# Kernel optimization log

Measured on AMD Instinct MI355X. Metric: run time of the kernel, lower is better.

## Reference

```python
import jax, jax.numpy as jnp
import numpy as np
from jax import lax

GROUPS = 32
EPS = 1e-5
NEG_SLOPE = 0.1


def group_norm(x, gamma, beta):
    # x: (B, C, H, W); GroupNorm over (C//G, H, W) per group
    B, C, H, W = x.shape
    xr = x.reshape(B, GROUPS, C // GROUPS, H, W)
    mean = xr.mean(axis=(2, 3, 4), keepdims=True)
    var = xr.var(axis=(2, 3, 4), keepdims=True)
    xn = ((xr - mean) * lax.rsqrt(var + EPS)).reshape(B, C, H, W)
    return xn * gamma[None, :, None, None] + beta[None, :, None, None]


def conv3x3(x, w, b):
    y = lax.conv_general_dilated(x, w, (1, 1), 'SAME',
                                 dimension_numbers=('NCHW', 'OIHW', 'NCHW'))
    return y + b[None, :, None, None]


def leaky_relu(x):
    return jnp.where(x >= 0, x, NEG_SLOPE * x)


def setup_inputs() -> dict:
    key = jax.random.key(0)
    ks = jax.random.split(key, 12)
    B, C, H, W = 16, 128, 128, 128
    emb = 128
    s = 0.05
    return {
        'x': jax.random.normal(ks[0], (B, C, H, W), jnp.float32),
        'time_emb': jax.random.normal(ks[1], (B, emb), jnp.float32),
        'k_v': jax.random.normal(ks[2], (B, 64), jnp.float32),
        'gn1_g': jnp.ones((C,), jnp.float32),
        'gn1_b': jnp.zeros((C,), jnp.float32),
        'conv1_w': jax.random.normal(ks[3], (C, C, 3, 3), jnp.float32) * s,
        'conv1_b': jax.random.normal(ks[4], (C,), jnp.float32) * s,
        'nf_w': jax.random.normal(ks[5], (C, emb), jnp.float32) * s,
        'nf_b': jax.random.normal(ks[6], (C,), jnp.float32) * s,
        'kW1': jax.random.normal(ks[7], (64, 64), jnp.float32) * s,
        'kW2': jax.random.normal(ks[8], (C * 9, 64), jnp.float32) * s,
        'daconv_w': jax.random.normal(ks[9], (C, C, 3, 3), jnp.float32) * s,
        'daconv_b': jax.random.normal(ks[10], (C,), jnp.float32) * s,
    }


def reference(x, time_emb, k_v, gn1_g, gn1_b, conv1_w, conv1_b,
              nf_w, nf_b, kW1, kW2, daconv_w, daconv_b):
    B, C, H, W = x.shape
    # block1: GroupNorm -> Swish -> Conv3x3
    h = group_norm(x, gn1_g, gn1_b)
    h = h * jax.nn.sigmoid(h)
    h = conv3x3(h, conv1_w, conv1_b)
    # FeatureWiseAffine (use_affine_level=False): h + Linear(time_emb)
    h = h + (time_emb @ nf_w.T + nf_b)[:, :, None, None]
    # DABlock: its GroupNorm+Swish output is discarded in the original code,
    # so only DA_conv(h, k_v) matters.
    # dynamic per-sample depthwise kernel: (B, 64) -> (B*C, 1, 3, 3)
    kern = (leaky_relu(k_v @ kW1.T) @ kW2.T).reshape(B * C, 1, 3, 3)
    xr = h.reshape(1, B * C, H, W)
    dyn = lax.conv_general_dilated(xr, kern, (1, 1), 'SAME',
                                   dimension_numbers=('NCHW', 'OIHW', 'NCHW'),
                                   feature_group_count=B * C)
    dyn = leaky_relu(dyn).reshape(B, C, H, W)
    h = dyn + conv3x3(h, daconv_w, daconv_b)
    # residual: dim == dim_out -> res_conv = Identity
    return h + x
```

## Files before the change

kernel.cpp:

```cpp
#include <hip/hip_runtime.h>
#include <hip/hip_bf16.h>
#include <math.h>
#include <stdint.h>

typedef unsigned short u16;
typedef __attribute__((ext_vector_type(8))) short bfrag;
typedef __attribute__((ext_vector_type(4))) float f32x4;
typedef __attribute__((ext_vector_type(8))) unsigned short u16x8;
typedef __attribute__((ext_vector_type(4))) unsigned short u16x4;

#define BB 16
#define CC 128
#define HH 128
#define WW 128
#define EPSV 1e-5f
#define NEG 0.1f
#define PW 130

__device__ __forceinline__ float bf2f(u16 u) {
    unsigned int x = ((unsigned int)u) << 16;
    return __builtin_bit_cast(float, x);
}
__device__ __forceinline__ u16 f2bf(float f) {
    unsigned int x = __builtin_bit_cast(unsigned int, f);
    unsigned int r = x + 0x7fffu + ((x >> 16) & 1u);
    return (u16)(r >> 16);
}
__device__ __forceinline__ void gload_lds16(const void* g, void* l) {
    __builtin_amdgcn_global_load_lds(
        (const __attribute__((address_space(1))) void*)g,
        (__attribute__((address_space(3))) void*)l, 16, 0, 0);
}

__global__ __launch_bounds__(256)
void border_kernel(u16* __restrict__ a, u16* __restrict__ h) {
    int idx = blockIdx.x * 256 + threadIdx.x;
    if (idx >= BB * 516 * 16) return;
    int cg = idx & 15;
    int t = idx >> 4;
    int b = t / 516, e = t - b * 516;
    int y, x;
    if (e < 130)      { y = 0;           x = e; }
    else if (e < 260) { y = 129;         x = e - 130; }
    else if (e < 388) { y = e - 260 + 1; x = 0; }
    else              { y = e - 388 + 1; x = 129; }
    size_t o = (((size_t)b * PW + y) * PW + x) * 128 + cg * 8;
    u16x8 z = (u16x8)(u16)0;
    *(u16x8*)&a[o] = z;
    *(u16x8*)&h[o] = z;
}

__global__ __launch_bounds__(256)
void gn_stats_kernel(const float* __restrict__ x, float* __restrict__ stats) {
    const int bg = blockIdx.x;
    const float* base = x + (size_t)bg * 65536;
    float s1 = 0.f, s2 = 0.f;
    for (int i = threadIdx.x; i < 16384; i += 256) {
        float4 v = *(const float4*)&base[i * 4];
        s1 += v.x + v.y + v.z + v.w;
        s2 += v.x * v.x + v.y * v.y + v.z * v.z + v.w * v.w;
    }
    #pragma unroll
    for (int off = 32; off > 0; off >>= 1) {
        s1 += __shfl_down(s1, off);
        s2 += __shfl_down(s2, off);
    }
    __shared__ float rs[8];
    const int wid = threadIdx.x >> 6, lane = threadIdx.x & 63;
    if (lane == 0) { rs[wid * 2] = s1; rs[wid * 2 + 1] = s2; }
    __syncthreads();
    if (threadIdx.x == 0) {
        s1 = rs[0] + rs[2] + rs[4] + rs[6];
        s2 = rs[1] + rs[3] + rs[5] + rs[7];
        float mean = s1 * (1.f / 65536.f);
        float var  = s2 * (1.f / 65536.f) - mean * mean;
        stats[2 * bg]     = mean;
        stats[2 * bg + 1] = rsqrtf(var + EPSV);
    }
}

__global__ __launch_bounds__(256)
void wconv_kernel(const float* __restrict__ w1, const float* __restrict__ w2,
                  u16* __restrict__ w1t, u16* __restrict__ w2t) {
    int idx = blockIdx.x * 256 + threadIdx.x;
    if (idx < 147456) {
        int e  = idx & 7;
        int co = (idx >> 3) & 127;
        int g  = (idx >> 10) & 3;
        int ck = (idx >> 12) & 3;
        int t  = idx >> 14;
        int src = (co * 128 + (ck * 32 + g * 8 + e)) * 9 + t;
        w1t[idx] = f2bf(w1[src]);
        w2t[idx] = f2bf(w2[src]);
    }
}

__global__ __launch_bounds__(256)
void small1_kernel(const float* __restrict__ te, const float* __restrict__ nfw,
                   const float* __restrict__ nfbias, const float* __restrict__ c1b,
                   const float* __restrict__ kv, const float* __restrict__ kw1,
                   float* __restrict__ biastot, float* __restrict__ tmp1) {
    const int idx = blockIdx.x * 256 + threadIdx.x;
    if (idx < 1024) {
        const int b = idx >> 6, j = idx & 63;
        float s = 0.f;
        for (int e = 0; e < 64; ++e) s += kv[b * 64 + e] * kw1[j * 64 + e];
        tmp1[idx] = s >= 0.f ? s : NEG * s;
    } else if (idx < 1024 + 2048) {
        const int t = idx - 1024;
        const int b = t >> 7, c = t & 127;
        float s = nfbias[c] + c1b[c];
        for (int e = 0; e < 128; ++e) s += te[b * 128 + e] * nfw[c * 128 + e];
        biastot[t] = s;
    }
}

__global__ __launch_bounds__(256)
void small2_kernel(const float* __restrict__ tmp1, const float* __restrict__ kw2,
                   float* __restrict__ kern_t) {
    const int idx = blockIdx.x * 256 + threadIdx.x;
    if (idx < BB * CC * 9) {
        const int b = idx / 1152, rc = idx % 1152;
        const int c = rc / 9, t = rc - c * 9;
        float s = 0.f;
        for (int e = 0; e < 64; ++e) s += tmp1[b * 64 + e] * kw2[rc * 64 + e];
        kern_t[((size_t)b * 9 + t) * 128 + c] = s;
    }
}

__global__ __launch_bounds__(256)
void gn_apply_kernel(const float* __restrict__ x, const float* __restrict__ gamma,
                     const float* __restrict__ beta, const float* __restrict__ stats,
                     u16* __restrict__ hact) {
    __shared__ u16 s_t[128 * 128];
    const int tid = threadIdx.x;
    const int y = blockIdx.x & 127, b = blockIdx.x >> 7;
    #pragma unroll
    for (int i = 0; i < 16; ++i) {
        int unit = (i << 8) + tid;
        int c = unit >> 5, xq = unit & 31, xx = xq * 4;
        float4 v = *(const float4*)&x[(((size_t)b * 128 + c) * 128 + y) * 128 + xx];
        int gi = b * 32 + (c >> 2);
        float mean = stats[2 * gi], rstd = stats[2 * gi + 1];
        float ga = gamma[c] * rstd, be = beta[c] - mean * ga;
        float a0 = v.x * ga + be, a1 = v.y * ga + be, a2 = v.z * ga + be, a3 = v.w * ga + be;
        a0 = a0 / (1.f + __expf(-a0)); a1 = a1 / (1.f + __expf(-a1));
        a2 = a2 / (1.f + __expf(-a2)); a3 = a3 / (1.f + __expf(-a3));
        int cs = c ^ ((xq & 15) << 3);
        s_t[(xx + 0) * 128 + cs] = f2bf(a0);
        s_t[(xx + 1) * 128 + cs] = f2bf(a1);
        s_t[(xx + 2) * 128 + cs] = f2bf(a2);
        s_t[(xx + 3) * 128 + cs] = f2bf(a3);
    }
    __syncthreads();
    #pragma unroll
    for (int i = 0; i < 8; ++i) {
        int unit = (i << 8) + tid;
        int xx = unit >> 4, c0 = (unit & 15) * 8;
        int c0s = c0 ^ (((xx >> 2) & 15) << 3);
        u16x8 v = *(const u16x8*)&s_t[xx * 128 + c0s];
        *(u16x8*)&hact[(((size_t)b * PW + y + 1) * PW + (xx + 1)) * 128 + c0] = v;
    }
}

template <int FINAL>
__global__ __launch_bounds__(512, 2)
void conv_mfma_kernel(const u16* __restrict__ act, const u16* __restrict__ wt,
                      const float* __restrict__ bias, const float* __restrict__ kern_t,
                      const float* __restrict__ xres,
                      float* __restrict__ outf, u16* __restrict__ outh) {
    __shared__ __align__(16) u16 s_in[2][1536 * 8];
    __shared__ float s_k[1152];

    const int tid = threadIdx.x;
    const int lane = tid & 63, wid = tid >> 6;
    const int wm = wid & 1, wq = wid >> 1;
    const int l15 = lane & 15, l4 = lane >> 4;

    const int bid0 = blockIdx.x;
    const int bid = ((bid0 & 7) << 7) | (bid0 >> 3);
    const int tx = bid & 7, ty = (bid >> 3) & 7, b = bid >> 6;
    const int x0 = tx * 16, y0 = ty * 16;

    f32x4 acc[4][4];
    #pragma unroll
    for (int mi = 0; mi < 4; ++mi)
        #pragma unroll
        for (int nj = 0; nj < 4; ++nj) acc[mi][nj] = (f32x4)(0.f);

    float dw[2][2][4][4];
    if constexpr (FINAL) {
        #pragma unroll
        for (int a0 = 0; a0 < 2; ++a0)
            #pragma unroll
            for (int a1 = 0; a1 < 2; ++a1)
                #pragma unroll
                for (int a2 = 0; a2 < 4; ++a2)
                    #pragma unroll
                    for (int a3 = 0; a3 < 4; ++a3) dw[a0][a1][a2][a3] = 0.f;
        for (int i = tid; i < 1152; i += 512) s_k[i] = kern_t[(size_t)b * 1152 + i];
        __syncthreads();
    }

    int in_vofs[3];
    #pragma unroll
    for (int r = 0; r < 3; ++r) {
        int slot = r * 512 + tid;
        int cik = slot / 384;
        int pos = slot - cik * 384;
        if (pos > 323) pos = 323;
        int row = pos / 18, col = pos - row * 18;
        in_vofs[r] = (row * PW + col) * 128 + cik * 8;
    }
    const u16* in_base = act + (((size_t)b * PW + y0) * PW + x0) * 128;
    const int ldst = (wid << 6) * 8;

    auto stage_in = [&](int buf, int ci0) {
        #pragma unroll
        for (int r = 0; r < 3; ++r)
            gload_lds16(in_base + ci0 + in_vofs[r], &s_in[buf][r * 512 * 8 + ldst]);
    };

    const u16* wlane = wt + l4 * 1024 + (wm * 64 + l15) * 8;
    const int bbase = (l4 * 384 + (wq * 4) * 18 + l15) * 8;

    auto dwcomp = [&](int ck, int dyr) {
        if constexpr (FINAL) {
            if ((ck >> 1) == wm) {
                const int mih = ck & 1;
                const u16* sb = &s_in[ck & 1][0];
                #pragma unroll
                for (int mm = 0; mm < 2; ++mm) {
                    const int cik = 2 * mm + (l4 >> 1);
                    const int e0 = (l4 & 1) * 4;
                    const int cb = ck * 32 + mm * 16 + l4 * 4;
                    #pragma unroll
                    for (int dx = 0; dx < 3; ++dx) {
                        const int tap = dyr * 3 + dx;
                        float4 kk = *(const float4*)&s_k[tap * 128 + cb];
                        #pragma unroll
                        for (int nj = 0; nj < 4; ++nj) {
                            const int row = wq * 4 + nj + dyr;
                            const int col = l15 + dx;
                            u16x4 hv = *(const u16x4*)
                                &sb[(cik * 384 + row * 18 + col) * 8 + e0];
                            dw[mih][mm][nj][0] += bf2f(hv[0]) * kk.x;
                            dw[mih][mm][nj][1] += bf2f(hv[1]) * kk.y;
                            dw[mih][mm][nj][2] += bf2f(hv[2]) * kk.z;
                            dw[mih][mm][nj][3] += bf2f(hv[3]) * kk.w;
                        }
                    }
                }
            }
        }
    };

    stage_in(0, 0);
    asm volatile("s_waitcnt vmcnt(0)" ::: "memory");
    __builtin_amdgcn_s_barrier();
    __builtin_amdgcn_sched_barrier(0);

    #pragma unroll
    for (int c = 0; c < 4; ++c) {
        if (c > 0) {
            __builtin_amdgcn_s_barrier();
        }
        if (c < 3) {
            stage_in((c + 1) & 1, (c + 1) * 32);
            asm volatile("s_waitcnt vmcnt(3)" ::: "memory");
        }
        __builtin_amdgcn_sched_barrier(0);

        const u16* sb = &s_in[c & 1][0];
        #pragma unroll
        for (int dyr = 0; dyr < 3; ++dyr) {
            bfrag wR[3][4];
            #pragma unroll
            for (int dx = 0; dx < 3; ++dx) {
                const u16* wp = wlane + ((dyr * 3 + dx) * 4 + c) * 4096;
                #pragma unroll
                for (int mi = 0; mi < 4; ++mi)
                    wR[dx][mi] = *(const bfrag*)(wp + mi * 128);
            }
            __builtin_amdgcn_s_setprio(1);
            #pragma unroll
            for (int dx = 0; dx < 3; ++dx) {
                const int bo = bbase + (dyr * 18 + dx) * 8;
                bfrag b0 = *(const bfrag*)&sb[bo];
                bfrag b1 = *(const bfrag*)&sb[bo + 144];
                bfrag b2 = *(const bfrag*)&sb[bo + 288];
                bfrag b3 = *(const bfrag*)&sb[bo + 432];

                acc[0][0] = __builtin_amdgcn_mfma_f32_16x16x32_bf16(wR[dx][0], b0, acc[0][0], 0, 0, 0);
                acc[0][1] = __builtin_amdgcn_mfma_f32_16x16x32_bf16(wR[dx][0], b1, acc[0][1], 0, 0, 0);
                acc[0][2] = __builtin_amdgcn_mfma_f32_16x16x32_bf16(wR[dx][0], b2, acc[0][2], 0, 0, 0);
                acc[0][3] = __builtin_amdgcn_mfma_f32_16x16x32_bf16(wR[dx][0], b3, acc[0][3], 0, 0, 0);
                acc[1][0] = __builtin_amdgcn_mfma_f32_16x16x32_bf16(wR[dx][1], b0, acc[1][0], 0, 0, 0);
                acc[1][1] = __builtin_amdgcn_mfma_f32_16x16x32_bf16(wR[dx][1], b1, acc[1][1], 0, 0, 0);
                acc[1][2] = __builtin_amdgcn_mfma_f32_16x16x32_bf16(wR[dx][1], b2, acc[1][2], 0, 0, 0);
                acc[1][3] = __builtin_amdgcn_mfma_f32_16x16x32_bf16(wR[dx][1], b3, acc[1][3], 0, 0, 0);
                acc[2][0] = __builtin_amdgcn_mfma_f32_16x16x32_bf16(wR[dx][2], b0, acc[2][0], 0, 0, 0);
                acc[2][1] = __builtin_amdgcn_mfma_f32_16x16x32_bf16(wR[dx][2], b1, acc[2][1], 0, 0, 0);
                acc[2][2] = __builtin_amdgcn_mfma_f32_16x16x32_bf16(wR[dx][2], b2, acc[2][2], 0, 0, 0);
                acc[2][3] = __builtin_amdgcn_mfma_f32_16x16x32_bf16(wR[dx][2], b3, acc[2][3], 0, 0, 0);
                acc[3][0] = __builtin_amdgcn_mfma_f32_16x16x32_bf16(wR[dx][3], b0, acc[3][0], 0, 0, 0);
                acc[3][1] = __builtin_amdgcn_mfma_f32_16x16x32_bf16(wR[dx][3], b1, acc[3][1], 0, 0, 0);
                acc[3][2] = __builtin_amdgcn_mfma_f32_16x16x32_bf16(wR[dx][3], b2, acc[3][2], 0, 0, 0);
                acc[3][3] = __builtin_amdgcn_mfma_f32_16x16x32_bf16(wR[dx][3], b3, acc[3][3], 0, 0, 0);
            }
            __builtin_amdgcn_s_setprio(0);
            dwcomp(c, dyr);
        }
    }

    if (!FINAL) {
        const float* bb = bias + b * 128;
        #pragma unroll
        for (int mi = 0; mi < 4; ++mi) {
            const int cb = wm * 64 + mi * 16 + l4 * 4;
            float4 bv4 = *(const float4*)&bb[cb];
            #pragma unroll
            for (int nj = 0; nj < 4; ++nj) {
                int y = y0 + wq * 4 + nj, xx = x0 + l15;
                u16x4 pk;
                pk[0] = f2bf(acc[mi][nj][0] + bv4.x);
                pk[1] = f2bf(acc[mi][nj][1] + bv4.y);
                pk[2] = f2bf(acc[mi][nj][2] + bv4.z);
                pk[3] = f2bf(acc[mi][nj][3] + bv4.w);
                *(u16x4*)&outh[(((size_t)b * PW + y + 1) * PW + (xx + 1)) * 128 + cb] = pk;
            }
        }
    } else {
        #pragma unroll
        for (int mi = 0; mi < 4; ++mi) {
            const int cb = wm * 64 + mi * 16 + l4 * 4;
            float4 bv4 = *(const float4*)&bias[cb];
            #pragma unroll
            for (int nj = 0; nj < 4; ++nj) {
                int y = y0 + wq * 4 + nj, xx = x0 + l15;
                size_t obase = (((size_t)b * 128 + cb) * 128 + y) * 128 + xx;
                #pragma unroll
                for (int j = 0; j < 4; ++j) {
                    float d = dw[mi >> 1][mi & 1][nj][j];
                    d = d >= 0.f ? d : NEG * d;
                    float bj = (j == 0) ? bv4.x : (j == 1) ? bv4.y : (j == 2) ? bv4.z : bv4.w;
                    outf[obase + (size_t)j * 16384] =
                        acc[mi][nj][j] + bj + d + xres[obase + (size_t)j * 16384];
                }
            }
        }
    }
}

extern "C" void kernel_launch(void* const* d_in, const int* in_sizes, int n_in,
                              void* d_out, int out_size, void* d_ws, size_t ws_size,
                              hipStream_t stream) {
    const float* x        = (const float*)d_in[0];
    const float* te       = (const float*)d_in[1];
    const float* kv       = (const float*)d_in[2];
    const float* gn1_g    = (const float*)d_in[3];
    const float* gn1_b    = (const float*)d_in[4];
    const float* conv1_w  = (const float*)d_in[5];
    const float* conv1_b  = (const float*)d_in[6];
    const float* nf_w     = (const float*)d_in[7];
    const float* nf_b     = (const float*)d_in[8];
    const float* kW1      = (const float*)d_in[9];
    const float* kW2      = (const float*)d_in[10];
    const float* daconv_w = (const float*)d_in[11];
    const float* daconv_b = (const float*)d_in[12];

    float* out = (float*)d_out;

    float* kern  = (float*)d_ws;
    u16*   w2t   = (u16*)(kern + 18432);
    u16*   hbuf  = (u16*)(kern + 92160);

    u16*   hact    = (u16*)out;
    float* up      = out + 17500160;
    float* stats   = up;
    float* biastot = up + 1024;
    float* tmp1    = up + 3072;
    u16*   w1t     = (u16*)(up + 4096);

    border_kernel<<<dim3(516), dim3(256), 0, stream>>>(hact, hbuf);
    gn_stats_kernel<<<dim3(512), dim3(256), 0, stream>>>(x, stats);
    wconv_kernel<<<dim3(576), dim3(256), 0, stream>>>(conv1_w, daconv_w, w1t, w2t);
    small1_kernel<<<dim3(12), dim3(256), 0, stream>>>(te, nf_w, nf_b, conv1_b, kv, kW1,
                                                      biastot, tmp1);
    small2_kernel<<<dim3(72), dim3(256), 0, stream>>>(tmp1, kW2, kern);
    gn_apply_kernel<<<dim3(2048), dim3(256), 0, stream>>>(x, gn1_g, gn1_b, stats, hact);

    conv_mfma_kernel<0><<<dim3(1024), dim3(512), 0, stream>>>(
        hact, w1t, biastot, nullptr, nullptr, nullptr, hbuf);
    conv_mfma_kernel<1><<<dim3(1024), dim3(512), 0, stream>>>(
        hbuf, w2t, daconv_b, kern, x, out, nullptr);
}
```

Baseline: 316.0 us.

## Split conv kernels and give conv1 taller 32-row tiles with 1024-thread blocks

Replaces the templated conv kernel with two separate kernels. conv1 now uses 1024-thread blocks, each covering a 32x16 spatial tile, so the 3x3 halo rows are reloaded less often relative to the output area. It reads weight fragments straight from global memory for every tap. conv2 keeps the original tiling and dynamic depthwise fusion, with some dead index code. The larger tile raises LDS use per block, and the aggressive launch bounds may limit registers and occupancy.

```diff
diff --git a/kernel.cpp b/kernel.cpp
--- a/kernel.cpp
+++ b/kernel.cpp
@@ -163,14 +163,10 @@
     }
 }
 
-template <int FINAL>
-__global__ __launch_bounds__(512, 2)
-void conv_mfma_kernel(const u16* __restrict__ act, const u16* __restrict__ wt,
-                      const float* __restrict__ bias, const float* __restrict__ kern_t,
-                      const float* __restrict__ xres,
-                      float* __restrict__ outf, u16* __restrict__ outh) {
-    __shared__ __align__(16) u16 s_in[2][1536 * 8];
-    __shared__ float s_k[1152];
+__global__ __launch_bounds__(1024, 4)
+void conv1_mfma_kernel(const u16* __restrict__ act, const u16* __restrict__ wt,
+                       const float* __restrict__ bias, u16* __restrict__ outh) {
+    __shared__ __align__(16) u16 s_in[2][2496 * 8];
 
     const int tid = threadIdx.x;
     const int lane = tid & 63, wid = tid >> 6;
@@ -178,9 +174,131 @@
     const int l15 = lane & 15, l4 = lane >> 4;
 
     const int bid0 = blockIdx.x;
+    const int bid = ((bid0 & 7) << 6) | (bid0 >> 3);
+    const int tx = bid & 7, ty = (bid >> 3) & 3, b = bid >> 5;
+    const int x0 = tx * 16, y0 = ty * 32;
+
+    f32x4 acc[4][4];
+    #pragma unroll
+    for (int mi = 0; mi < 4; ++mi)
+        #pragma unroll
+        for (int nj = 0; nj < 4; ++nj) acc[mi][nj] = (f32x4)(0.f);
+
+    int in_vofs[3];
+    bool in_act[3];
+    #pragma unroll
+    for (int r = 0; r < 3; ++r) {
+        int slot_base = r * 1024 + (wid << 6);
+        in_act[r] = slot_base < 2448;
+        int slot = r * 1024 + tid;
+        if (slot > 2447) slot = 2447;
+        int cik = slot / 612;
+        int pos = slot - cik * 612;
+        int row = pos / 18, col = pos - row * 18;
+        in_vofs[r] = (row * PW + col) * 128 + cik * 8;
+    }
+    const u16* in_base = act + (((size_t)b * PW + y0) * PW + x0) * 128;
+    const int ldst = (wid << 6) * 8;
+
+    auto stage_in = [&](int buf, int ci0) {
+        #pragma unroll
+        for (int r = 0; r < 3; ++r)
+            if (in_act[r])
+                gload_lds16(in_base + ci0 + in_vofs[r],
+                            &s_in[buf][(r * 1024) * 8 + ldst]);
+    };
+
+    const u16* wlane = wt + l4 * 1024 + (wm * 64 + l15) * 8;
+    const int bbase = (l4 * 612 + (wq * 4) * 18 + l15) * 8;
+
+    stage_in(0, 0);
+    asm volatile("s_waitcnt vmcnt(0)" ::: "memory");
+    __builtin_amdgcn_s_barrier();
+    __builtin_amdgcn_sched_barrier(0);
+
+    #pragma unroll
+    for (int c = 0; c < 4; ++c) {
+        if (c > 0) {
+            asm volatile("s_waitcnt vmcnt(0)" ::: "memory");
+            __builtin_amdgcn_s_barrier();
+        }
+        if (c < 3) stage_in((c + 1) & 1, (c + 1) * 32);
+        __builtin_amdgcn_sched_barrier(0);
+
+        const u16* sb = &s_in[c & 1][0];
+        #pragma unroll
+        for (int dyr = 0; dyr < 3; ++dyr) {
+            #pragma unroll
+            for (int dx = 0; dx < 3; ++dx) {
+                const u16* wp = wlane + ((dyr * 3 + dx) * 4 + c) * 4096;
+                bfrag a0 = *(const bfrag*)(wp);
+                bfrag a1 = *(const bfrag*)(wp + 128);
+                bfrag a2 = *(const bfrag*)(wp + 256);
+                bfrag a3 = *(const bfrag*)(wp + 384);
+                const int bo = bbase + (dyr * 18 + dx) * 8;
+                bfrag b0 = *(const bfrag*)&sb[bo];
+                bfrag b1 = *(const bfrag*)&sb[bo + 144];
+                bfrag b2 = *(const bfrag*)&sb[bo + 288];
+                bfrag b3 = *(const bfrag*)&sb[bo + 432];
+
+                __builtin_amdgcn_s_setprio(1);
+                acc[0][0] = __builtin_amdgcn_mfma_f32_16x16x32_bf16(a0, b0, acc[0][0], 0, 0, 0);
+                acc[0][1] = __builtin_amdgcn_mfma_f32_16x16x32_bf16(a0, b1, acc[0][1], 0, 0, 0);
+                acc[0][2] = __builtin_amdgcn_mfma_f32_16x16x32_bf16(a0, b2, acc[0][2], 0, 0, 0);
+                acc[0][3] = __builtin_amdgcn_mfma_f32_16x16x32_bf16(a0, b3, acc[0][3], 0, 0, 0);
+                acc[1][0] = __builtin_amdgcn_mfma_f32_16x16x32_bf16(a1, b0, acc[1][0], 0, 0, 0);
+                acc[1][1] = __builtin_amdgcn_mfma_f32_16x16x32_bf16(a1, b1, acc[1][1], 0, 0, 0);
+                acc[1][2] = __builtin_amdgcn_mfma_f32_16x16x32_bf16(a1, b2, acc[1][2], 0, 0, 0);
+                acc[1][3] = __builtin_amdgcn_mfma_f32_16x16x32_bf16(a1, b3, acc[1][3], 0, 0, 0);
+                acc[2][0] = __builtin_amdgcn_mfma_f32_16x16x32_bf16(a2, b0, acc[2][0], 0, 0, 0);
+                acc[2][1] = __builtin_amdgcn_mfma_f32_16x16x32_bf16(a2, b1, acc[2][1], 0, 0, 0);
+                acc[2][2] = __builtin_amdgcn_mfma_f32_16x16x32_bf16(a2, b2, acc[2][2], 0, 0, 0);
+                acc[2][3] = __builtin_amdgcn_mfma_f32_16x16x32_bf16(a2, b3, acc[2][3], 0, 0, 0);
+                acc[3][0] = __builtin_amdgcn_mfma_f32_16x16x32_bf16(a3, b0, acc[3][0], 0, 0, 0);
+                acc[3][1] = __builtin_amdgcn_mfma_f32_16x16x32_bf16(a3, b1, acc[3][1], 0, 0, 0);
+                acc[3][2] = __builtin_amdgcn_mfma_f32_16x16x32_bf16(a3, b2, acc[3][2], 0, 0, 0);
+                acc[3][3] = __builtin_amdgcn_mfma_f32_16x16x32_bf16(a3, b3, acc[3][3], 0, 0, 0);
+                __builtin_amdgcn_s_setprio(0);
+            }
+        }
+    }
+
+    const float* bb = bias + b * 128;
+    #pragma unroll
+    for (int mi = 0; mi < 4; ++mi) {
+        const int cb = wm * 64 + mi * 16 + l4 * 4;
+        float4 bv4 = *(const float4*)&bb[cb];
+        #pragma unroll
+        for (int nj = 0; nj < 4; ++nj) {
+            int y = y0 + wq * 4 + nj, xx = x0 + l15;
+            u16x4 pk;
+            pk[0] = f2bf(acc[mi][nj][0] + bv4.x);
+            pk[1] = f2bf(acc[mi][nj][1] + bv4.y);
+            pk[2] = f2bf(acc[mi][nj][2] + bv4.z);
+            pk[3] = f2bf(acc[mi][nj][3] + bv4.w);
+            *(u16x4*)&outh[(((size_t)b * PW + y + 1) * PW + (xx + 1)) * 128 + cb] = pk;
+        }
+    }
+}
+
+__global__ __launch_bounds__(512, 2)
+void conv2_mfma_kernel(const u16* __restrict__ act, const u16* __restrict__ wt,
+                       const float* __restrict__ bias, const float* __restrict__ kern_t,
+                       const float* __restrict__ xres, float* __restrict__ outf) {
+    __shared__ __align__(16) u16 s_in[2][1536 * 8];
+    __shared__ float s_k[1152];
+
+    const int tid = threadIdx.x;
+    const int lane = tid & 63, wid = tid >> 6;
+    const int wm = wid & 1, wq = wid >> 1;
+    const int l15 = lane & 15, l4 = lane >> 4;
+
+    const int bid0 = blockIdx.x;
     const int bid = ((bid0 & 7) << 7) | (bid0 >> 3);
-    const int tx = bid & 7, ty = (bid >> 3) & 7, b = bid >> 6;
-    const int x0 = tx * 16, y0 = ty * 16;
+    const int tx = bid & 7, ty = (bid >> 3) & 15, b = bid >> 7;
+    const int x0 = tx * 16, y0 = (ty & 7) * 16;
+    const int b2 = bid >> 6;
+    (void)b2;
 
     f32x4 acc[4][4];
     #pragma unroll
@@ -189,18 +307,22 @@
         for (int nj = 0; nj < 4; ++nj) acc[mi][nj] = (f32x4)(0.f);
 
     float dw[2][2][4][4];
-    if constexpr (FINAL) {
-        #pragma unroll
-        for (int a0 = 0; a0 < 2; ++a0)
-            #pragma unroll
-            for (int a1 = 0; a1 < 2; ++a1)
+    #pragma unroll
+    for (int a0 = 0; a0 < 2; ++a0)
+        #pragma unroll
+        for (int a1 = 0; a1 < 2; ++a1)
+            #pragma unroll
+            for (int a2 = 0; a2 < 4; ++a2)
                 #pragma unroll
-                for (int a2 = 0; a2 < 4; ++a2)
-                    #pragma unroll
-                    for (int a3 = 0; a3 < 4; ++a3) dw[a0][a1][a2][a3] = 0.f;
-        for (int i = tid; i < 1152; i += 512) s_k[i] = kern_t[(size_t)b * 1152 + i];
-        __syncthreads();
-    }
+                for (int a3 = 0; a3 < 4; ++a3) dw[a0][a1][a2][a3] = 0.f;
+
+    const int bb_ = bid >> 6;
+    const int b_  = bb_;
+    const int ty_ = (bid >> 3) & 7;
+    const int y0_ = ty_ * 16;
+
+    for (int i = tid; i < 1152; i += 512) s_k[i] = kern_t[(size_t)b_ * 1152 + i];
+    __syncthreads();
 
     int in_vofs[3];
     #pragma unroll
@@ -212,7 +334,7 @@
         int row = pos / 18, col = pos - row * 18;
         in_vofs[r] = (row * PW + col) * 128 + cik * 8;
     }
-    const u16* in_base = act + (((size_t)b * PW + y0) * PW + x0) * 128;
+    const u16* in_base = act + (((size_t)b_ * PW + y0_) * PW + x0) * 128;
     const int ldst = (wid << 6) * 8;
 
     auto stage_in = [&](int buf, int ci0) {
@@ -225,30 +347,28 @@
     const int bbase = (l4 * 384 + (wq * 4) * 18 + l15) * 8;
 
     auto dwcomp = [&](int ck, int dyr) {
-        if constexpr (FINAL) {
-            if ((ck >> 1) == wm) {
-                const int mih = ck & 1;
-                const u16* sb = &s_in[ck & 1][0];
+        if ((ck >> 1) == wm) {
+            const int mih = ck & 1;
+            const u16* sb = &s_in[ck & 1][0];
+            #pragma unroll
+            for (int mm = 0; mm < 2; ++mm) {
+                const int cik = 2 * mm + (l4 >> 1);
+                const int e0 = (l4 & 1) * 4;
+                const int cb = ck * 32 + mm * 16 + l4 * 4;
                 #pragma unroll
-                for (int mm = 0; mm < 2; ++mm) {
-                    const int cik = 2 * mm + (l4 >> 1);
-                    const int e0 = (l4 & 1) * 4;
-                    const int cb = ck * 32 + mm * 16 + l4 * 4;
+                for (int dx = 0; dx < 3; ++dx) {
+                    const int tap = dyr * 3 + dx;
+                    float4 kk = *(const float4*)&s_k[tap * 128 + cb];
                     #pragma unroll
-                    for (int dx = 0; dx < 3; ++dx) {
-                        const int tap = dyr * 3 + dx;
-                        float4 kk = *(const float4*)&s_k[tap * 128 + cb];
-                        #pragma unroll
-                        for (int nj = 0; nj < 4; ++nj) {
-                            const int row = wq * 4 + nj + dyr;
-                            const int col = l15 + dx;
-                            u16x4 hv = *(const u16x4*)
-                                &sb[(cik * 384 + row * 18 + col) * 8 + e0];
-                            dw[mih][mm][nj][0] += bf2f(hv[0]) * kk.x;
-                            dw[mih][mm][nj][1] += bf2f(hv[1]) * kk.y;
-                            dw[mih][mm][nj][2] += bf2f(hv[2]) * kk.z;
-                            dw[mih][mm][nj][3] += bf2f(hv[3]) * kk.w;
-                        }
+                    for (int nj = 0; nj < 4; ++nj) {
+                        const int row = wq * 4 + nj + dyr;
+                        const int col = l15 + dx;
+                        u16x4 hv = *(const u16x4*)
+                            &sb[(cik * 384 + row * 18 + col) * 8 + e0];
+                        dw[mih][mm][nj][0] += bf2f(hv[0]) * kk.x;
+                        dw[mih][mm][nj][1] += bf2f(hv[1]) * kk.y;
+                        dw[mih][mm][nj][2] += bf2f(hv[2]) * kk.z;
+                        dw[mih][mm][nj][3] += bf2f(hv[3]) * kk.w;
                     }
                 }
             }
@@ -313,40 +433,21 @@
         }
     }
 
-    if (!FINAL) {
-        const float* bb = bias + b * 128;
-        #pragma unroll
-        for (int mi = 0; mi < 4; ++mi) {
-            const int cb = wm * 64 + mi * 16 + l4 * 4;
-            float4 bv4 = *(const float4*)&bb[cb];
-            #pragma unroll
-            for (int nj = 0; nj < 4; ++nj) {
-                int y = y0 + wq * 4 + nj, xx = x0 + l15;
-                u16x4 pk;
-                pk[0] = f2bf(acc[mi][nj][0] + bv4.x);
-                pk[1] = f2bf(acc[mi][nj][1] + bv4.y);
-                pk[2] = f2bf(acc[mi][nj][2] + bv4.z);
-                pk[3] = f2bf(acc[mi][nj][3] + bv4.w);
-                *(u16x4*)&outh[(((size_t)b * PW + y + 1) * PW + (xx + 1)) * 128 + cb] = pk;
-            }
-        }
-    } else {
-        #pragma unroll
-        for (int mi = 0; mi < 4; ++mi) {
-            const int cb = wm * 64 + mi * 16 + l4 * 4;
-            float4 bv4 = *(const float4*)&bias[cb];
-            #pragma unroll
-            for (int nj = 0; nj < 4; ++nj) {
-                int y = y0 + wq * 4 + nj, xx = x0 + l15;
-                size_t obase = (((size_t)b * 128 + cb) * 128 + y) * 128 + xx;
-                #pragma unroll
-                for (int j = 0; j < 4; ++j) {
-                    float d = dw[mi >> 1][mi & 1][nj][j];
-                    d = d >= 0.f ? d : NEG * d;
-                    float bj = (j == 0) ? bv4.x : (j == 1) ? bv4.y : (j == 2) ? bv4.z : bv4.w;
-                    outf[obase + (size_t)j * 16384] =
-                        acc[mi][nj][j] + bj + d + xres[obase + (size_t)j * 16384];
-                }
+    #pragma unroll
+    for (int mi = 0; mi < 4; ++mi) {
+        const int cb = wm * 64 + mi * 16 + l4 * 4;
+        float4 bv4 = *(const float4*)&bias[cb];
+        #pragma unroll
+        for (int nj = 0; nj < 4; ++nj) {
+            int y = y0_ + wq * 4 + nj, xx = x0 + l15;
+            size_t obase = (((size_t)b_ * 128 + cb) * 128 + y) * 128 + xx;
+            #pragma unroll
+            for (int j = 0; j < 4; ++j) {
+                float d = dw[mi >> 1][mi & 1][nj][j];
+                d = d >= 0.f ? d : NEG * d;
+                float bj = (j == 0) ? bv4.x : (j == 1) ? bv4.y : (j == 2) ? bv4.z : bv4.w;
+                outf[obase + (size_t)j * 16384] =
+                    acc[mi][nj][j] + bj + d + xres[obase + (size_t)j * 16384];
             }
         }
     }
@@ -390,8 +491,7 @@
     small2_kernel<<<dim3(72), dim3(256), 0, stream>>>(tmp1, kW2, kern);
     gn_apply_kernel<<<dim3(2048), dim3(256), 0, stream>>>(x, gn1_g, gn1_b, stats, hact);
 
-    conv_mfma_kernel<0><<<dim3(1024), dim3(512), 0, stream>>>(
-        hact, w1t, biastot, nullptr, nullptr, nullptr, hbuf);
-    conv_mfma_kernel<1><<<dim3(1024), dim3(512), 0, stream>>>(
-        hbuf, w2t, daconv_b, kern, x, out, nullptr);
-}
+    conv1_mfma_kernel<<<dim3(512), dim3(1024), 0, stream>>>(hact, w1t, biastot, hbuf);
+    conv2_mfma_kernel<<<dim3(1024), dim3(512), 0, stream>>>(
+        hbuf, w2t, daconv_b, kern, x, out);
+}
```

Result: slower. 323.4 us (+2.3%).
